# Kernel tuning notes

Measured on AMD Instinct MI355X. Metric: run time of the kernel, lower is better.

Reference implementation:

```python
import jax, jax.numpy as jnp
import numpy as np

LENGTHS = [1024, 768, 896, 512, 1024, 640, 1024, 768, 512, 896, 1024, 704]  # sum = 9792
EMBED, HEADS = 1024, 16
HDIM = EMBED // HEADS  # 64
ROPE_BASE = 10000.0


def _rotate_half(x):
    half = x.shape[-1] // 2
    return jnp.concatenate([-x[..., half:], x[..., :half]], axis=-1)


def setup_inputs() -> dict:
    key = jax.random.key(0)
    ks = jax.random.split(key, 8)
    T = sum(LENGTHS)
    hidden = jax.random.normal(ks[0], (T, EMBED), jnp.float32)
    # RoPE cos/sin: positions restart at 0 within each packed segment
    pos = np.concatenate([np.arange(l) for l in LENGTHS]).astype(np.float32)  # [T]
    inv_freq = 1.0 / (ROPE_BASE ** (np.arange(0, HDIM, 2, dtype=np.float32) / HDIM))
    freqs = np.outer(pos, inv_freq)                       # [T, HDIM//2]
    emb = np.concatenate([freqs, freqs], axis=-1)         # [T, HDIM]
    cos = jnp.asarray(np.cos(emb), jnp.float32)
    sin = jnp.asarray(np.sin(emb), jnp.float32)
    s = 0.02
    q_w = jax.random.normal(ks[1], (EMBED, EMBED), jnp.float32) * s
    k_w = jax.random.normal(ks[2], (EMBED, EMBED), jnp.float32) * s
    v_w = jax.random.normal(ks[3], (EMBED, EMBED), jnp.float32) * s
    out_w = jax.random.normal(ks[4], (EMBED, EMBED), jnp.float32) * s
    q_b = jax.random.normal(ks[5], (EMBED,), jnp.float32) * s
    v_b = jax.random.normal(ks[6], (EMBED,), jnp.float32) * s
    out_b = jax.random.normal(ks[7], (EMBED,), jnp.float32) * s
    return {
        "hidden_states": hidden, "cos": cos, "sin": sin,
        "q_w": q_w, "q_b": q_b, "k_w": k_w, "v_w": v_w, "v_b": v_b,
        "out_w": out_w, "out_b": out_b,
        "seq_len": jnp.array(LENGTHS, jnp.int32),
        "max_seqlen": 1024,
    }


def reference(hidden_states, cos, sin, q_w, q_b, k_w, v_w, v_b, out_w, out_b,
              seq_len, max_seqlen):
    T, D = hidden_states.shape
    H, Dh = HEADS, D // HEADS
    B = seq_len.shape[0]
    L = max_seqlen  # static python int

    # Projections (torch Linear: y = x @ W.T + b; k_proj has no bias)
    q = (hidden_states @ q_w.T + q_b).reshape(T, H, Dh)
    k = (hidden_states @ k_w.T).reshape(T, H, Dh)
    v = (hidden_states @ v_w.T + v_b).reshape(T, H, Dh)

    # Inline RoPE (cos/sin broadcast over heads)
    c = cos[:, None, :]
    s = sin[:, None, :]
    q = q * c + _rotate_half(q) * s
    k = k * c + _rotate_half(k) * s

    # Gather packed tokens into padded [B, L, H, Dh] (honors ragged structure:
    # no [T, T] dense score matrix, only per-segment [L, L] blocks)
    cu = jnp.concatenate([jnp.zeros((1,), seq_len.dtype), jnp.cumsum(seq_len)])[:-1]  # [B] starts
    ar = jnp.arange(L)
    idx = cu[:, None] + ar[None, :]                 # [B, L] token ids
    valid = ar[None, :] < seq_len[:, None]          # [B, L]
    idxc = jnp.minimum(idx, T - 1)
    qp = q[idxc]                                    # [B, L, H, Dh]
    kp = k[idxc]
    vp = v[idxc]

    scale = 1.0 / jnp.sqrt(jnp.float32(Dh))
    scores = jnp.einsum('blhd,bmhd->bhlm', qp, kp) * scale  # [B, H, L, L]
    causal = ar[:, None] >= ar[None, :]             # [L, L]
    mask = valid[:, None, None, :] & causal[None, None, :, :]
    scores = jnp.where(mask, scores, jnp.float32(-1e30))
    probs = jax.nn.softmax(scores, axis=-1)
    attn = jnp.einsum('bhlm,bmhd->blhd', probs, vp).reshape(B, L, D)

    # Scatter valid tokens back to packed layout [T, D]
    attn = attn * valid[..., None].astype(attn.dtype)
    flat = jnp.zeros((T, D), attn.dtype).at[idxc.reshape(-1)].add(attn.reshape(-1, D))
    return flat @ out_w.T + out_b
```

## Files before the change

### kernel.cpp

```cpp
#include <hip/hip_runtime.h>

typedef __bf16 bf16;
typedef __bf16 bf16x8 __attribute__((ext_vector_type(8)));
typedef __bf16 bf16x4 __attribute__((ext_vector_type(4)));
typedef float  f32x4  __attribute__((ext_vector_type(4)));

#define T_TOTAL 9792
#define EMBED   1024
#define NHEAD   16
#define HDIM    64

__constant__ int c_seq_start[12] = {0,1024,1792,2688,3200,4224,4864,5888,6656,7168,8064,9088};
__constant__ int c_tiles_cum[13] = {0,16,28,42,50,66,76,92,104,112,126,142,153};

typedef __attribute__((address_space(1))) unsigned int gu32;
typedef __attribute__((address_space(3))) unsigned int lu32;

__device__ __forceinline__ void load_lds16(const void* g, void* l) {
    __builtin_amdgcn_global_load_lds((gu32*)g, (lu32*)l, 16, 0, 0);
}

__device__ __forceinline__ f32x4 mfma16(bf16x8 a, bf16x8 b, f32x4 c) {
    return __builtin_amdgcn_mfma_f32_16x16x32_bf16(a, b, c, 0, 0, 0);
}

__device__ __forceinline__ int xcd_chunk(int bid, int chunk) {
    return (bid & 7) * chunk + (bid >> 3);
}

struct CvtArgs {
    const void* src[10];
    bf16*       dst[10];
    int         n[10];
    int         cum[10];
};

__global__ void to_bf16_fused(CvtArgs a, const unsigned short* __restrict__ disc)
{
    const bool f32 = (disc[0] == 0);
    const int blk = blockIdx.x;
    int seg = 0;
    #pragma unroll
    for (int i = 1; i < 10; ++i) if (blk >= a.cum[i]) seg = i;
    int i0 = (blk - a.cum[seg]) * 2048 + threadIdx.x * 8;
    if (i0 >= a.n[seg]) return;
    bf16x8 o;
    if (f32) {
        const float4* s = (const float4*)((const float*)a.src[seg] + i0);
        float4 x = s[0], y = s[1];
        o[0]=(bf16)x.x; o[1]=(bf16)x.y; o[2]=(bf16)x.z; o[3]=(bf16)x.w;
        o[4]=(bf16)y.x; o[5]=(bf16)y.y; o[6]=(bf16)y.z; o[7]=(bf16)y.w;
    } else {
        o = *(const bf16x8*)((const bf16*)a.src[seg] + i0);
    }
    *(bf16x8*)(a.dst[seg] + i0) = o;
}

__device__ __forceinline__
void gemm_core(const bf16* __restrict__ A, const bf16* __restrict__ W,
               int M, int m0, int n0, f32x4 (&acc)[4][4],
               bf16* lA, bf16* lB)
{
    const int tid  = threadIdx.x;
    const int wave = tid >> 6, lane = tid & 63;
    const int lrow = lane >> 3;
    const int gsw  = (lane & 7) ^ lrow;
    const int ln   = lane & 15, lq = lane >> 4;
    const int e7   = ln & 7;
    const int wm = (wave & 1) * 64,  wn = (wave >> 1) * 64;

    for (int k0 = 0; k0 < 1024; k0 += 64) {
        __syncthreads();
        for (int j = 0; j < 4; ++j) {
            int r = j * 32 + wave * 8;
            int gr = m0 + r + lrow; if (gr > M - 1) gr = M - 1;
            load_lds16(A + (size_t)gr * EMBED + k0 + gsw * 8, &lA[r * 64]);
            load_lds16(W + (size_t)(n0 + r + lrow) * EMBED + k0 + gsw * 8, &lB[r * 64]);
        }
        __syncthreads();
        #pragma unroll
        for (int kb = 0; kb < 2; ++kb) {
            bf16x8 af[4], bfr[4];
            #pragma unroll
            for (int i = 0; i < 4; ++i)
                af[i]  = *(const bf16x8*)&lA[(wm + i * 16 + ln) * 64 + (((kb * 4 + lq) ^ e7) * 8)];
            #pragma unroll
            for (int i = 0; i < 4; ++i)
                bfr[i] = *(const bf16x8*)&lB[(wn + i * 16 + ln) * 64 + (((kb * 4 + lq) ^ e7) * 8)];
            #pragma unroll
            for (int mi = 0; mi < 4; ++mi)
                #pragma unroll
                for (int ni = 0; ni < 4; ++ni)
                    acc[mi][ni] = mfma16(af[mi], bfr[ni], acc[mi][ni]);
        }
    }
}

__device__ __forceinline__ void map_block(int L, int NY, int& x, int& y)
{
    const int per = 8 * NY;
    const int full = 9 * per;
    if (L < full) { int sc = L / per, rem = L % per; x = sc * 8 + (rem & 7); y = rem >> 3; }
    else          { int rem = L - full; x = 72 + rem % 5; y = rem / 5; }
}

__global__ __launch_bounds__(256, 2)
void gemm_qkv(const bf16* __restrict__ A,
              const bf16* __restrict__ Wq, const bf16* __restrict__ Wk,
              const bf16* __restrict__ Wv, const bf16* __restrict__ qb,
              const bf16* __restrict__ vb,
              const bf16* __restrict__ cosb, const bf16* __restrict__ sinb,
              bf16* __restrict__ Cq, bf16* __restrict__ Ck,
              bf16* __restrict__ Vt, int M)
{
    __shared__ __align__(16) bf16 lA[128 * 64];
    __shared__ __align__(16) bf16 lB[128 * 64];

    int x, yy;
    map_block(xcd_chunk(blockIdx.x, 231), 24, x, yy);
    const int which = yy >> 3;
    const int m0 = x * 128, n0 = (yy & 7) * 128;

    const bf16* W = (which == 0) ? Wq : (which == 1) ? Wk : Wv;
    f32x4 acc[4][4] = {};
    gemm_core(A, W, M, m0, n0, acc, lA, lB);

    const int tid  = threadIdx.x;
    const int wave = tid >> 6, lane = tid & 63;
    const int ln   = lane & 15, lq = lane >> 4;
    const int wm = (wave & 1) * 64,  wn = (wave >> 1) * 64;

    if (which < 2) {
        bf16* C = (which == 0) ? Cq : Ck;
        const bf16* bias = (which == 0) ? qb : nullptr;
        #pragma unroll
        for (int mi = 0; mi < 4; ++mi) {
            int trow = m0 + wm + mi * 16 + lq * 4;
            if (trow >= M) continue;
            #pragma unroll
            for (int ni = 0; ni < 2; ++ni) {
                int d    = ni * 16 + ln;
                int col0 = n0 + wn + d;
                int col1 = col0 + 32;
                float b0 = bias ? (float)bias[col0] : 0.0f;
                float b1 = bias ? (float)bias[col1] : 0.0f;
                #pragma unroll
                for (int r = 0; r < 4; ++r) {
                    int t = trow + r;
                    float c = (float)cosb[t * HDIM + d];
                    float s = (float)sinb[t * HDIM + d];
                    float x0 = acc[mi][ni][r] + b0;
                    float x1 = acc[mi][ni + 2][r] + b1;
                    C[(size_t)t * EMBED + col0] = (bf16)(x0 * c - x1 * s);
                    C[(size_t)t * EMBED + col1] = (bf16)(x1 * c + x0 * s);
                }
            }
        }
    } else {
        const int hd0 = n0 + wn;
        #pragma unroll
        for (int mi = 0; mi < 4; ++mi) {
            int trow = m0 + wm + mi * 16 + lq * 4;
            if (trow >= M) continue;
            #pragma unroll
            for (int ni = 0; ni < 4; ++ni) {
                int d = ni * 16 + ln;
                float bv = (float)vb[hd0 + d];
                bf16x4 o;
                #pragma unroll
                for (int r = 0; r < 4; ++r) o[r] = (bf16)(acc[mi][ni][r] + bv);
                *(bf16x4*)&Vt[(size_t)(hd0 + d) * T_TOTAL + trow] = o;
            }
        }
    }
}

__global__ __launch_bounds__(256, 2)
void gemm_out(const bf16* __restrict__ A, const bf16* __restrict__ W,
              const bf16* __restrict__ bias, void* __restrict__ out, int M,
              const unsigned short* __restrict__ disc)
{
    __shared__ __align__(16) bf16 lA[128 * 64];
    __shared__ __align__(16) bf16 lB[128 * 64];

    int x, yy;
    map_block(xcd_chunk(blockIdx.x, 77), 8, x, yy);
    const int m0 = x * 128, n0 = yy * 128;

    f32x4 acc[4][4] = {};
    gemm_core(A, W, M, m0, n0, acc, lA, lB);

    const bool f32 = (disc[0] == 0);
    const int tid  = threadIdx.x;
    const int wave = tid >> 6, lane = tid & 63;
    const int ln   = lane & 15, lq = lane >> 4;
    const int wm = (wave & 1) * 64,  wn = (wave >> 1) * 64;

    #pragma unroll
    for (int mi = 0; mi < 4; ++mi) {
        int trow = m0 + wm + mi * 16 + lq * 4;
        if (trow >= M) continue;
        #pragma unroll
        for (int ni = 0; ni < 4; ++ni) {
            int col = n0 + wn + ni * 16 + ln;
            float bv = (float)bias[col];
            #pragma unroll
            for (int r = 0; r < 4; ++r) {
                float v = acc[mi][ni][r] + bv;
                size_t idx = (size_t)(trow + r) * EMBED + col;
                if (f32) ((float*)out)[idx] = v;
                else     ((bf16*)out)[idx]  = (bf16)v;
            }
        }
    }
}

__global__ __launch_bounds__(256, 3)
void attn_kernel(const bf16* __restrict__ Q, const bf16* __restrict__ K,
                 const bf16* __restrict__ Vt, bf16* __restrict__ O)
{
    __shared__ __align__(16) bf16 sK[2][64 * 64];
    __shared__ __align__(16) bf16 sV[2][64 * 64];
    __shared__ __align__(16) bf16 sQP[4 * 16 * 72];

    const int tid  = threadIdx.x;
    const int wave = tid >> 6, lane = tid & 63;
    const int lrow = lane >> 3;
    const int gsw  = (lane & 7) ^ lrow;
    const int ln   = lane & 15, lq = lane >> 4;
    const int e7   = ln & 7;

    const int swz = xcd_chunk(blockIdx.x, 306);
    const int h  = swz / 153;
    const int qx = swz - h * 153;

    int b = 0;
    #pragma unroll
    for (int i = 1; i < 13; ++i) if (qx >= c_tiles_cum[i]) b = i;
    const int qt = qx - c_tiles_cum[b];
    const int t0 = c_seq_start[b] + qt * 64;
    const int kvb0 = c_seq_start[b];

    for (int p = 0; p < 2; ++p) {
        int r = p * 32 + wave * 8;
        load_lds16(Q  + (size_t)(t0 + r + lrow) * EMBED + h * HDIM + gsw * 8, &sQP[r * 64]);
        load_lds16(K  + (size_t)(kvb0 + r + lrow) * EMBED + h * HDIM + gsw * 8, &sK[0][r * 64]);
        load_lds16(Vt + (size_t)(h * HDIM + r + lrow) * T_TOTAL + kvb0 + gsw * 8, &sV[0][r * 64]);
    }

    bf16x8 qf[2];
    f32x4 oacc[4] = {};
    float m_i = -1e30f, l_i = 0.0f;
    const float sc = 0.125f * 1.44269504088896f;
    const int q_loc = wave * 16 + ln;
    bf16* sP = &sQP[wave * 16 * 72];

    for (int j = 0; j <= qt; ++j) {
        __syncthreads();
        const int cur = j & 1;
        if (j == 0) {
            qf[0] = *(const bf16x8*)&sQP[q_loc * 64 + ((0 + lq) ^ e7) * 8];
            qf[1] = *(const bf16x8*)&sQP[q_loc * 64 + ((4 + lq) ^ e7) * 8];
            __syncthreads();
        }
        if (j < qt) {
            const int kvb = kvb0 + (j + 1) * 64;
            const int nxt = cur ^ 1;
            for (int p = 0; p < 2; ++p) {
                int r = p * 32 + wave * 8;
                load_lds16(K  + (size_t)(kvb + r + lrow) * EMBED + h * HDIM + gsw * 8, &sK[nxt][r * 64]);
                load_lds16(Vt + (size_t)(h * HDIM + r + lrow) * T_TOTAL + kvb + gsw * 8, &sV[nxt][r * 64]);
            }
        }

        f32x4 s[4] = {};
        #pragma unroll
        for (int kk = 0; kk < 2; ++kk)
            #pragma unroll
            for (int ni = 0; ni < 4; ++ni) {
                bf16x8 kf = *(const bf16x8*)&sK[cur][(ni * 16 + ln) * 64 + (((kk * 4 + lq) ^ e7) * 8)];
                s[ni] = mfma16(kf, qf[kk], s[ni]);
            }

        float pb[4][4];
        if (j == qt) {
            #pragma unroll
            for (int ni = 0; ni < 4; ++ni)
                #pragma unroll
                for (int r = 0; r < 4; ++r) {
                    int kv = ni * 16 + lq * 4 + r;
                    pb[ni][r] = (kv <= q_loc) ? s[ni][r] * sc : -1e30f;
                }
        } else {
            #pragma unroll
            for (int ni = 0; ni < 4; ++ni)
                #pragma unroll
                for (int r = 0; r < 4; ++r)
                    pb[ni][r] = s[ni][r] * sc;
        }

        float mx = pb[0][0];
        #pragma unroll
        for (int ni = 0; ni < 4; ++ni)
            #pragma unroll
            for (int r = 0; r < 4; ++r) mx = fmaxf(mx, pb[ni][r]);
        mx = fmaxf(mx, __shfl_xor(mx, 16));
        mx = fmaxf(mx, __shfl_xor(mx, 32));

        if (!__all(mx <= m_i + 8.0f)) {
            float mnew  = fmaxf(m_i, mx);
            float alpha = exp2f(m_i - mnew);
            l_i *= alpha;
            #pragma unroll
            for (int d = 0; d < 4; ++d)
                #pragma unroll
                for (int r = 0; r < 4; ++r) oacc[d][r] *= alpha;
            m_i = mnew;
        }

        float rs = 0.0f;
        #pragma unroll
        for (int ni = 0; ni < 4; ++ni)
            #pragma unroll
            for (int r = 0; r < 4; ++r) {
                float pe = exp2f(pb[ni][r] - m_i);
                pb[ni][r] = pe;
                rs += pe;
            }
        rs += __shfl_xor(rs, 16);
        rs += __shfl_xor(rs, 32);
        l_i += rs;

        #pragma unroll
        for (int ni = 0; ni < 4; ++ni) {
            bf16x4 w4;
            #pragma unroll
            for (int r = 0; r < 4; ++r) w4[r] = (bf16)pb[ni][r];
            *(bf16x4*)&sP[ln * 72 + ni * 16 + lq * 4] = w4;
        }
        asm volatile("s_waitcnt lgkmcnt(0)" ::: "memory");

        #pragma unroll
        for (int kk = 0; kk < 2; ++kk) {
            bf16x8 pf = *(const bf16x8*)&sP[ln * 72 + kk * 32 + lq * 8];
            #pragma unroll
            for (int d = 0; d < 4; ++d) {
                bf16x8 vf = *(const bf16x8*)&sV[cur][(d * 16 + ln) * 64 + (((kk * 4 + lq) ^ e7) * 8)];
                oacc[d] = mfma16(vf, pf, oacc[d]);
            }
        }
    }

    const float inv = 1.0f / l_i;
    const size_t row = (size_t)(t0 + q_loc) * EMBED + h * HDIM;
    #pragma unroll
    for (int d = 0; d < 4; ++d) {
        bf16x4 o4;
        #pragma unroll
        for (int r = 0; r < 4; ++r) o4[r] = (bf16)(oacc[d][r] * inv);
        *(bf16x4*)&O[row + d * 16 + lq * 4] = o4;
    }
}

extern "C" void kernel_launch(void* const* d_in, const int* in_sizes, int n_in,
                              void* d_out, int out_size, void* d_ws, size_t ws_size,
                              hipStream_t stream)
{
    const unsigned short* disc = (const unsigned short*)d_in[1];

    const size_t SZ  = (size_t)T_TOTAL * EMBED;
    const size_t CS  = (size_t)T_TOTAL * HDIM;
    const size_t WSZ = (size_t)EMBED * EMBED;

    bf16* p = (bf16*)d_ws;
    bf16* ch   = p; p += SZ;
    bf16* ccos = p; p += CS;
    bf16* csin = p; p += CS;
    bf16* cqw  = p; p += WSZ;
    bf16* ckw  = p; p += WSZ;
    bf16* cvw  = p; p += WSZ;
    bf16* cow  = p; p += WSZ;
    bf16* cqb  = p; p += EMBED;
    bf16* cvb  = p; p += EMBED;
    bf16* cob  = p; p += EMBED;
    bf16* wq   = p; p += SZ;
    bf16* wk   = p; p += SZ;
    bf16* wvt  = p; p += SZ;

    CvtArgs ca;
    const void* srcs[10] = {d_in[0], d_in[1], d_in[2], d_in[3], d_in[5],
                            d_in[6], d_in[8], d_in[4], d_in[7], d_in[9]};
    bf16* dsts[10] = {ch, ccos, csin, cqw, ckw, cvw, cow, cqb, cvb, cob};
    int   ns[10]   = {(int)SZ, (int)CS, (int)CS, (int)WSZ, (int)WSZ,
                      (int)WSZ, (int)WSZ, EMBED, EMBED, EMBED};
    int cum = 0;
    for (int i = 0; i < 10; ++i) {
        ca.src[i] = srcs[i]; ca.dst[i] = dsts[i]; ca.n[i] = ns[i];
        ca.cum[i] = cum;
        cum += (ns[i] + 2047) / 2048;
    }
    to_bf16_fused<<<cum, 256, 0, stream>>>(ca, disc);

    gemm_qkv<<<77 * 24, 256, 0, stream>>>(ch, cqw, ckw, cvw, cqb, cvb,
                                          ccos, csin, wq, wk, wvt, T_TOTAL);
    attn_kernel<<<2448, 256, 0, stream>>>(wq, wk, wvt, wq);
    gemm_out<<<77 * 8, 256, 0, stream>>>(wq, cow, cob, d_out, T_TOTAL, disc);
}
```

Baseline: 286.4 us.

## Double-buffer GEMM K-loop with BK=32 stages and one barrier per step

```diff
diff --git a/kernel.cpp b/kernel.cpp
--- a/kernel.cpp
+++ b/kernel.cpp
@@ -58,41 +58,55 @@
 
 __device__ __forceinline__
 void gemm_core(const bf16* __restrict__ A, const bf16* __restrict__ W,
-               int M, int m0, int n0, f32x4 (&acc)[4][4],
-               bf16* lA, bf16* lB)
+               int M, int m0, int n0, f32x4 (&acc)[4][4], bf16* lds)
 {
     const int tid  = threadIdx.x;
     const int wave = tid >> 6, lane = tid & 63;
-    const int lrow = lane >> 3;
-    const int gsw  = (lane & 7) ^ lrow;
     const int ln   = lane & 15, lq = lane >> 4;
-    const int e7   = ln & 7;
-    const int wm = (wave & 1) * 64,  wn = (wave >> 1) * 64;
-
-    for (int k0 = 0; k0 < 1024; k0 += 64) {
-        __syncthreads();
-        for (int j = 0; j < 4; ++j) {
-            int r = j * 32 + wave * 8;
-            int gr = m0 + r + lrow; if (gr > M - 1) gr = M - 1;
-            load_lds16(A + (size_t)gr * EMBED + k0 + gsw * 8, &lA[r * 64]);
-            load_lds16(W + (size_t)(n0 + r + lrow) * EMBED + k0 + gsw * 8, &lB[r * 64]);
-        }
-        __syncthreads();
-        #pragma unroll
-        for (int kb = 0; kb < 2; ++kb) {
-            bf16x8 af[4], bfr[4];
-            #pragma unroll
-            for (int i = 0; i < 4; ++i)
-                af[i]  = *(const bf16x8*)&lA[(wm + i * 16 + ln) * 64 + (((kb * 4 + lq) ^ e7) * 8)];
-            #pragma unroll
-            for (int i = 0; i < 4; ++i)
-                bfr[i] = *(const bf16x8*)&lB[(wn + i * 16 + ln) * 64 + (((kb * 4 + lq) ^ e7) * 8)];
-            #pragma unroll
-            for (int mi = 0; mi < 4; ++mi)
-                #pragma unroll
-                for (int ni = 0; ni < 4; ++ni)
-                    acc[mi][ni] = mfma16(af[mi], bfr[ni], acc[mi][ni]);
-        }
+    const int wm   = (wave & 1) * 64, wn = (wave >> 1) * 64;
+
+    const int srow = lane >> 2;
+    const int sg   = ((lane & 3) ^ (srow & 3)) * 8;
+
+    auto stage = [&](int t) {
+        const int k0 = t * 32;
+        bf16* dA = lds + (t & 1) * 8192;
+        bf16* dB = dA + 4096;
+        #pragma unroll
+        for (int j = 0; j < 2; ++j) {
+            int r = j * 64 + wave * 16;
+            int gra = m0 + r + srow; if (gra > M - 1) gra = M - 1;
+            load_lds16(A + (size_t)gra * EMBED + k0 + sg, &dA[r * 32]);
+            load_lds16(W + (size_t)(n0 + r + srow) * EMBED + k0 + sg, &dB[r * 32]);
+        }
+    };
+
+    stage(0);
+
+    const int rg = (lq ^ (ln & 3)) * 8;
+
+    for (int t = 0; t < 32; ++t) {
+        asm volatile("s_waitcnt vmcnt(0)" ::: "memory");
+        __builtin_amdgcn_s_barrier();
+        if (t + 1 < 32) stage(t + 1);
+
+        const bf16* sA = lds + (t & 1) * 8192;
+        const bf16* sB = sA + 4096;
+        bf16x8 af[4], bfr[4];
+        #pragma unroll
+        for (int i = 0; i < 4; ++i)
+            af[i]  = *(const bf16x8*)&sA[(wm + i * 16 + ln) * 32 + rg];
+        #pragma unroll
+        for (int i = 0; i < 4; ++i)
+            bfr[i] = *(const bf16x8*)&sB[(wn + i * 16 + ln) * 32 + rg];
+
+        __builtin_amdgcn_s_setprio(1);
+        #pragma unroll
+        for (int mi = 0; mi < 4; ++mi)
+            #pragma unroll
+            for (int ni = 0; ni < 4; ++ni)
+                acc[mi][ni] = mfma16(af[mi], bfr[ni], acc[mi][ni]);
+        __builtin_amdgcn_s_setprio(0);
     }
 }
 
@@ -113,8 +127,7 @@
               bf16* __restrict__ Cq, bf16* __restrict__ Ck,
               bf16* __restrict__ Vt, int M)
 {
-    __shared__ __align__(16) bf16 lA[128 * 64];
-    __shared__ __align__(16) bf16 lB[128 * 64];
+    __shared__ __align__(16) bf16 lds[2 * 8192];
 
     int x, yy;
     map_block(xcd_chunk(blockIdx.x, 231), 24, x, yy);
@@ -123,7 +136,7 @@
 
     const bf16* W = (which == 0) ? Wq : (which == 1) ? Wk : Wv;
     f32x4 acc[4][4] = {};
-    gemm_core(A, W, M, m0, n0, acc, lA, lB);
+    gemm_core(A, W, M, m0, n0, acc, lds);
 
     const int tid  = threadIdx.x;
     const int wave = tid >> 6, lane = tid & 63;
@@ -180,15 +193,14 @@
               const bf16* __restrict__ bias, void* __restrict__ out, int M,
               const unsigned short* __restrict__ disc)
 {
-    __shared__ __align__(16) bf16 lA[128 * 64];
-    __shared__ __align__(16) bf16 lB[128 * 64];
+    __shared__ __align__(16) bf16 lds[2 * 8192];
 
     int x, yy;
     map_block(xcd_chunk(blockIdx.x, 77), 8, x, yy);
     const int m0 = x * 128, n0 = yy * 128;
 
     f32x4 acc[4][4] = {};
-    gemm_core(A, W, M, m0, n0, acc, lA, lB);
+    gemm_core(A, W, M, m0, n0, acc, lds);
 
     const bool f32 = (disc[0] == 0);
     const int tid  = threadIdx.x;
```

Measured after the change: 290.9 us. Within noise of the previous version (+1.6%).

## Use 128-row query tiles with 8 waves sharing each K/V tile in attention

Applied to the files above, without the earlier changes.

```diff
diff --git a/kernel.cpp b/kernel.cpp
--- a/kernel.cpp
+++ b/kernel.cpp
@@ -10,8 +10,8 @@
 #define NHEAD   16
 #define HDIM    64
 
-__constant__ int c_seq_start[12] = {0,1024,1792,2688,3200,4224,4864,5888,6656,7168,8064,9088};
-__constant__ int c_tiles_cum[13] = {0,16,28,42,50,66,76,92,104,112,126,142,153};
+__constant__ int c_seq_start13[13] = {0,1024,1792,2688,3200,4224,4864,5888,6656,7168,8064,9088,9792};
+__constant__ int c_qtiles_cum[13] = {0,8,14,21,25,33,38,46,52,56,63,71,77};
 
 typedef __attribute__((address_space(1))) unsigned int gu32;
 typedef __attribute__((address_space(3))) unsigned int lu32;
@@ -215,13 +215,13 @@
     }
 }
 
-__global__ __launch_bounds__(256, 3)
+__global__ __launch_bounds__(512, 6)
 void attn_kernel(const bf16* __restrict__ Q, const bf16* __restrict__ K,
                  const bf16* __restrict__ Vt, bf16* __restrict__ O)
 {
     __shared__ __align__(16) bf16 sK[2][64 * 64];
     __shared__ __align__(16) bf16 sV[2][64 * 64];
-    __shared__ __align__(16) bf16 sQP[4 * 16 * 72];
+    __shared__ __align__(16) bf16 sQP[8 * 16 * 72];
 
     const int tid  = threadIdx.x;
     const int wave = tid >> 6, lane = tid & 63;
@@ -230,22 +230,30 @@
     const int ln   = lane & 15, lq = lane >> 4;
     const int e7   = ln & 7;
 
-    const int swz = xcd_chunk(blockIdx.x, 306);
-    const int h  = swz / 153;
-    const int qx = swz - h * 153;
+    const int swz = xcd_chunk(blockIdx.x, 154);
+    const int h  = swz / 77;
+    const int qx = swz - h * 77;
 
     int b = 0;
     #pragma unroll
-    for (int i = 1; i < 13; ++i) if (qx >= c_tiles_cum[i]) b = i;
-    const int qt = qx - c_tiles_cum[b];
-    const int t0 = c_seq_start[b] + qt * 64;
-    const int kvb0 = c_seq_start[b];
+    for (int i = 1; i < 13; ++i) if (qx >= c_qtiles_cum[i]) b = i;
+    const int qt   = qx - c_qtiles_cum[b];
+    const int s0   = c_seq_start13[b];
+    const int len  = c_seq_start13[b + 1] - s0;
+    const int t0   = s0 + qt * 128;
+    const int vrows = len - qt * 128;
+    const int lastrow = (vrows < 128 ? vrows : 128) - 1;
+    const int jmax = (qt * 128 + lastrow) >> 6;
 
     for (int p = 0; p < 2; ++p) {
-        int r = p * 32 + wave * 8;
-        load_lds16(Q  + (size_t)(t0 + r + lrow) * EMBED + h * HDIM + gsw * 8, &sQP[r * 64]);
-        load_lds16(K  + (size_t)(kvb0 + r + lrow) * EMBED + h * HDIM + gsw * 8, &sK[0][r * 64]);
-        load_lds16(Vt + (size_t)(h * HDIM + r + lrow) * T_TOTAL + kvb0 + gsw * 8, &sV[0][r * 64]);
+        int r = p * 64 + wave * 8 + lrow;
+        int qr = t0 + r; if (qr > T_TOTAL - 1) qr = T_TOTAL - 1;
+        load_lds16(Q + (size_t)qr * EMBED + h * HDIM + gsw * 8, &sQP[r * 64]);
+    }
+    {
+        int r = wave * 8 + lrow;
+        load_lds16(K  + (size_t)(s0 + r) * EMBED + h * HDIM + gsw * 8, &sK[0][r * 64]);
+        load_lds16(Vt + (size_t)(h * HDIM + r) * T_TOTAL + s0 + gsw * 8, &sV[0][r * 64]);
     }
 
     bf16x8 qf[2];
@@ -255,7 +263,7 @@
     const int q_loc = wave * 16 + ln;
     bf16* sP = &sQP[wave * 16 * 72];
 
-    for (int j = 0; j <= qt; ++j) {
+    for (int j = 0; j <= jmax; ++j) {
         __syncthreads();
         const int cur = j & 1;
         if (j == 0) {
@@ -263,14 +271,12 @@
             qf[1] = *(const bf16x8*)&sQP[q_loc * 64 + ((4 + lq) ^ e7) * 8];
             __syncthreads();
         }
-        if (j < qt) {
-            const int kvb = kvb0 + (j + 1) * 64;
+        if (j < jmax) {
+            const int kvb = s0 + (j + 1) * 64;
             const int nxt = cur ^ 1;
-            for (int p = 0; p < 2; ++p) {
-                int r = p * 32 + wave * 8;
-                load_lds16(K  + (size_t)(kvb + r + lrow) * EMBED + h * HDIM + gsw * 8, &sK[nxt][r * 64]);
-                load_lds16(Vt + (size_t)(h * HDIM + r + lrow) * T_TOTAL + kvb + gsw * 8, &sV[nxt][r * 64]);
-            }
+            int r = wave * 8 + lrow;
+            load_lds16(K  + (size_t)(kvb + r) * EMBED + h * HDIM + gsw * 8, &sK[nxt][r * 64]);
+            load_lds16(Vt + (size_t)(h * HDIM + r) * T_TOTAL + kvb + gsw * 8, &sV[nxt][r * 64]);
         }
 
         f32x4 s[4] = {};
@@ -283,12 +289,13 @@
             }
 
         float pb[4][4];
-        if (j == qt) {
+        if (j >= 2 * qt) {
+            const int off = (j - 2 * qt) * 64;
             #pragma unroll
             for (int ni = 0; ni < 4; ++ni)
                 #pragma unroll
                 for (int r = 0; r < 4; ++r) {
-                    int kv = ni * 16 + lq * 4 + r;
+                    int kv = off + ni * 16 + lq * 4 + r;
                     pb[ni][r] = (kv <= q_loc) ? s[ni][r] * sc : -1e30f;
                 }
         } else {
@@ -351,14 +358,16 @@
         }
     }
 
-    const float inv = 1.0f / l_i;
-    const size_t row = (size_t)(t0 + q_loc) * EMBED + h * HDIM;
-    #pragma unroll
-    for (int d = 0; d < 4; ++d) {
-        bf16x4 o4;
-        #pragma unroll
-        for (int r = 0; r < 4; ++r) o4[r] = (bf16)(oacc[d][r] * inv);
-        *(bf16x4*)&O[row + d * 16 + lq * 4] = o4;
+    if (q_loc < vrows) {
+        const float inv = 1.0f / l_i;
+        const size_t row = (size_t)(t0 + q_loc) * EMBED + h * HDIM;
+        #pragma unroll
+        for (int d = 0; d < 4; ++d) {
+            bf16x4 o4;
+            #pragma unroll
+            for (int r = 0; r < 4; ++r) o4[r] = (bf16)(oacc[d][r] * inv);
+            *(bf16x4*)&O[row + d * 16 + lq * 4] = o4;
+        }
     }
 }
 
@@ -403,6 +412,6 @@
 
     gemm_qkv<<<77 * 24, 256, 0, stream>>>(ch, cqw, ckw, cvw, cqb, cvb,
                                           ccos, csin, wq, wk, wvt, T_TOTAL);
-    attn_kernel<<<2448, 256, 0, stream>>>(wq, wk, wvt, wq);
+    attn_kernel<<<1232, 512, 0, stream>>>(wq, wk, wvt, wq);
     gemm_out<<<77 * 8, 256, 0, stream>>>(wq, cow, cob, d_out, T_TOTAL, disc);
 }
```

Measured after the change: 287.8 us. No clear change (+0.5%).
